# Kernel optimization log

Measured on AMD Instinct MI355X. Metric: run time of the kernel, lower is better.

## Reference

```python
import jax, jax.numpy as jnp
import numpy as np

NUM_HEADS = 12
LN_EPS = 1e-5


def _layernorm(x, w, b):
    m = jnp.mean(x, axis=-1, keepdims=True)
    v = jnp.mean(jnp.square(x - m), axis=-1, keepdims=True)
    return (x - m) * jax.lax.rsqrt(v + LN_EPS) * w + b


def setup_inputs() -> dict:
    key = jax.random.key(0)
    ks = jax.random.split(key, 6)
    B, N, C, H = 8, 1024, 768, 3072
    s = 0.02
    return {
        "x": jax.random.normal(ks[0], (B, N, C), jnp.float32),
        "ln1_w": jnp.ones((C,), jnp.float32),
        "ln1_b": jnp.zeros((C,), jnp.float32),
        "qkv_w": jax.random.normal(ks[1], (3 * C, C), jnp.float32) * s,
        "qkv_b": jnp.zeros((3 * C,), jnp.float32),
        "proj_w": jax.random.normal(ks[2], (C, C), jnp.float32) * s,
        "proj_b": jnp.zeros((C,), jnp.float32),
        "ln2_w": jnp.ones((C,), jnp.float32),
        "ln2_b": jnp.zeros((C,), jnp.float32),
        "fc1_w": jax.random.normal(ks[3], (H, C), jnp.float32) * s,
        "fc1_b": jnp.zeros((H,), jnp.float32),
        "fc2_w": jax.random.normal(ks[4], (C, H), jnp.float32) * s,
        "fc2_b": jnp.zeros((C,), jnp.float32),
    }


def reference(x, ln1_w, ln1_b, qkv_w, qkv_b, proj_w, proj_b,
              ln2_w, ln2_b, fc1_w, fc1_b, fc2_w, fc2_b):
    B, N, C = x.shape
    H = NUM_HEADS
    d = C // H
    scale = d ** (-0.5)

    # --- attention on norm1(x) (size=None path, dropout rates are 0) ---
    h = _layernorm(x, ln1_w, ln1_b)
    qkv = h @ qkv_w.T + qkv_b                      # [B,N,3C]
    qkv = qkv.reshape(B, N, 3, H, d).transpose(2, 0, 3, 1, 4)  # [3,B,H,N,d]
    q, k, v = qkv[0], qkv[1], qkv[2]
    attn = jnp.einsum('bhqd,bhkd->bhqk', q, k) * scale
    attn = jax.nn.softmax(attn, axis=-1)
    o = jnp.einsum('bhqk,bhkd->bhqd', attn, v)     # [B,H,N,d]
    o = o.transpose(0, 2, 1, 3).reshape(B, N, C)
    x_attn = o @ proj_w.T + proj_b

    # --- residual + MLP ---
    x = x + x_attn
    h2 = _layernorm(x, ln2_w, ln2_b)
    h2 = jax.nn.gelu(h2 @ fc1_w.T + fc1_b, approximate=False)
    x = x + (h2 @ fc2_w.T + fc2_b)
    return x
```

## Files before the change

### kernel.cpp

```cpp
#include <hip/hip_runtime.h>
#include <cmath>

typedef __bf16 bf16;
typedef __bf16 bf16x8 __attribute__((ext_vector_type(8)));
typedef __bf16 bf16x4 __attribute__((ext_vector_type(4)));
typedef float floatx4 __attribute__((ext_vector_type(4)));

#define MFMA16(A, B, C) __builtin_amdgcn_mfma_f32_16x16x32_bf16((A), (B), (C), 0, 0, 0)

#define GLDS16(g, l)                                                   \
  __builtin_amdgcn_global_load_lds(                                    \
      (const __attribute__((address_space(1))) void*)(g),              \
      (__attribute__((address_space(3))) void*)(l), 16, 0, 0)

__global__ __launch_bounds__(256) void pre_kernel(
    const float* __restrict__ x, const float* __restrict__ g,
    const float* __restrict__ be, bf16* __restrict__ h1,
    const float* __restrict__ s0, bf16* __restrict__ d0, int n0,
    const float* __restrict__ s1, bf16* __restrict__ d1, int n1,
    const float* __restrict__ s2, bf16* __restrict__ d2, int n2,
    const float* __restrict__ s3, bf16* __restrict__ d3, int n3) {
  int bid = blockIdx.x;
  int t = threadIdx.x;
  if (bid < 8192) {
    const float* xr = x + (size_t)bid * 768;
    float v0 = xr[t], v1 = xr[t + 256], v2 = xr[t + 512];
    float s = v0 + v1 + v2;
    float s2 = v0 * v0 + v1 * v1 + v2 * v2;
#pragma unroll
    for (int o = 1; o < 64; o <<= 1) {
      s += __shfl_xor(s, o, 64);
      s2 += __shfl_xor(s2, o, 64);
    }
    __shared__ float red[8];
    int w = t >> 6, lane = t & 63;
    if (lane == 0) { red[w] = s; red[4 + w] = s2; }
    __syncthreads();
    float ts = red[0] + red[1] + red[2] + red[3];
    float ts2 = red[4] + red[5] + red[6] + red[7];
    float mean = ts * (1.0f / 768.0f);
    float var = ts2 * (1.0f / 768.0f) - mean * mean;
    float rstd = rsqrtf(var + 1e-5f);
    bf16* orow = h1 + (size_t)bid * 768;
    orow[t]       = (bf16)((v0 - mean) * rstd * g[t]       + be[t]);
    orow[t + 256] = (bf16)((v1 - mean) * rstd * g[t + 256] + be[t + 256]);
    orow[t + 512] = (bf16)((v2 - mean) * rstd * g[t + 512] + be[t + 512]);
    return;
  }
  int i = (bid - 8192) * 256 + t;
  const float* s;
  bf16* d;
  if (i < n0) { s = s0 + (size_t)i * 4; d = d0 + (size_t)i * 4; }
  else if ((i -= n0) < n1) { s = s1 + (size_t)i * 4; d = d1 + (size_t)i * 4; }
  else if ((i -= n1) < n2) { s = s2 + (size_t)i * 4; d = d2 + (size_t)i * 4; }
  else if ((i -= n2) < n3) { s = s3 + (size_t)i * 4; d = d3 + (size_t)i * 4; }
  else return;
  bf16x4 v;
  v[0] = (bf16)s[0]; v[1] = (bf16)s[1]; v[2] = (bf16)s[2]; v[3] = (bf16)s[3];
  *(bf16x4*)d = v;
}

__global__ __launch_bounds__(256) void ln_kernel(const float* __restrict__ x,
                                                 const float* __restrict__ g,
                                                 const float* __restrict__ be,
                                                 bf16* __restrict__ out) {
  int row = blockIdx.x;
  int t = threadIdx.x;
  const float* xr = x + (size_t)row * 768;
  float v0 = xr[t], v1 = xr[t + 256], v2 = xr[t + 512];
  float s = v0 + v1 + v2;
  float s2 = v0 * v0 + v1 * v1 + v2 * v2;
#pragma unroll
  for (int o = 1; o < 64; o <<= 1) {
    s += __shfl_xor(s, o, 64);
    s2 += __shfl_xor(s2, o, 64);
  }
  __shared__ float red[8];
  int w = t >> 6, lane = t & 63;
  if (lane == 0) { red[w] = s; red[4 + w] = s2; }
  __syncthreads();
  float ts = red[0] + red[1] + red[2] + red[3];
  float ts2 = red[4] + red[5] + red[6] + red[7];
  float mean = ts * (1.0f / 768.0f);
  float var = ts2 * (1.0f / 768.0f) - mean * mean;
  float rstd = rsqrtf(var + 1e-5f);
  bf16* orow = out + (size_t)row * 768;
  orow[t]       = (bf16)((v0 - mean) * rstd * g[t]       + be[t]);
  orow[t + 256] = (bf16)((v1 - mean) * rstd * g[t + 256] + be[t + 256]);
  orow[t + 512] = (bf16)((v2 - mean) * rstd * g[t + 512] + be[t + 512]);
}

constexpr int EP_BF16 = 0;
constexpr int EP_RES_F32 = 1;
constexpr int EP_GELU_BF16 = 2;

template <int EP, int NJ>
__global__ __launch_bounds__(256, 3) void gemm_bt(
    const bf16* __restrict__ A, const bf16* __restrict__ Bw,
    const float* __restrict__ bias, const float* __restrict__ resid,
    void* __restrict__ outp, int M, int N, int K) {
  __shared__ alignas(16) bf16 Asl[128 * 64];
  __shared__ alignas(16) bf16 Bsl[NJ * 32 * 64];
  int tid = threadIdx.x;
  int lane = tid & 63, w = tid >> 6;
  int wm = w >> 1, wn = w & 1;
  int q16 = lane & 15, quad = lane >> 4;
  int fid = blockIdx.x + gridDim.x * blockIdx.y;
  int nb = gridDim.x;
  int s = fid >> 3;
  int m0 = ((fid & 7) * (gridDim.y >> 3) + s / nb) * 128;
  int n0 = (s % nb) * (NJ * 32);

  floatx4 acc[4][NJ];
#pragma unroll
  for (int i = 0; i < 4; i++)
#pragma unroll
    for (int j = 0; j < NJ; j++) acc[i][j] = (floatx4){0.f, 0.f, 0.f, 0.f};

  int rIn = lane >> 3;
  int cg = (lane & 7) ^ rIn;
  const bf16* ag[4];
  const bf16* bg[NJ];
#pragma unroll
  for (int q = 0; q < 4; q++)
    ag[q] = A + (size_t)(m0 + (w * 4 + q) * 8 + rIn) * K + cg * 8;
#pragma unroll
  for (int q = 0; q < NJ; q++)
    bg[q] = Bw + (size_t)(n0 + (w * NJ + q) * 8 + rIn) * K + cg * 8;
  bf16* la = &Asl[w * 2048];
  bf16* lb = &Bsl[w * NJ * 512];

  int msel = q16 & 7;
  int offA[2][4], offB[2][NJ];
#pragma unroll
  for (int ks = 0; ks < 2; ks++) {
#pragma unroll
    for (int i = 0; i < 4; i++)
      offA[ks][i] = (wm * 64 + i * 16 + q16) * 64 + (((ks * 4 + quad) ^ msel)) * 8;
#pragma unroll
    for (int j = 0; j < NJ; j++)
      offB[ks][j] = (wn * 16 * NJ + j * 16 + q16) * 64 + (((ks * 4 + quad) ^ msel)) * 8;
  }

  for (int k0 = 0; k0 < K; k0 += 64) {
    __syncthreads();
#pragma unroll
    for (int q = 0; q < 4; q++) {
      GLDS16(ag[q], la + q * 512);
      ag[q] += 64;
    }
#pragma unroll
    for (int q = 0; q < NJ; q++) {
      GLDS16(bg[q], lb + q * 512);
      bg[q] += 64;
    }
    __syncthreads();
#pragma unroll
    for (int ks = 0; ks < 2; ks++) {
      bf16x8 af[4], bfr[NJ];
#pragma unroll
      for (int i = 0; i < 4; i++) af[i] = *(const bf16x8*)&Asl[offA[ks][i]];
#pragma unroll
      for (int j = 0; j < NJ; j++) bfr[j] = *(const bf16x8*)&Bsl[offB[ks][j]];
#pragma unroll
      for (int i = 0; i < 4; i++)
#pragma unroll
        for (int j = 0; j < NJ; j++) acc[i][j] = MFMA16(af[i], bfr[j], acc[i][j]);
    }
  }

#pragma unroll
  for (int i = 0; i < 4; i++) {
#pragma unroll
    for (int j = 0; j < NJ; j++) {
#pragma unroll
      for (int r = 0; r < 4; r++) {
        int m = m0 + wm * 64 + i * 16 + quad * 4 + r;
        int n = n0 + wn * 16 * NJ + j * 16 + q16;
        size_t idx = (size_t)m * N + n;
        float v = acc[i][j][r] + bias[n];
        if constexpr (EP == EP_BF16) {
          ((bf16*)outp)[idx] = (bf16)v;
        } else if constexpr (EP == EP_RES_F32) {
          ((float*)outp)[idx] = v + resid[idx];
        } else {
          float u = v * (2.3022083f + 0.1029443f * v * v);
          float e = __builtin_amdgcn_exp2f(-u);
          float gv = v * __builtin_amdgcn_rcpf(1.0f + e);
          ((bf16*)outp)[idx] = (bf16)gv;
        }
      }
    }
  }
}

__global__ __launch_bounds__(256, 3) void attn_kernel(const bf16* __restrict__ qkv,
                                                      bf16* __restrict__ o) {
  __shared__ alignas(16) bf16 Kl[2][32 * 64];
  __shared__ alignas(16) bf16 Vt[2][64 * 40];
  __shared__ alignas(16) bf16 Pl[4][2][16 * 40];
  int tid = threadIdx.x;
  int lane = tid & 63, w = tid >> 6;
  int q16 = lane & 15, quad = lane >> 4;
  int b = blockIdx.y / 12, h = blockIdx.y % 12;
  int qbase = blockIdx.x * 128 + w * 32;
  const int KS = 32 * 2304;

  bf16x8 qf[2][2];
#pragma unroll
  for (int qt = 0; qt < 2; qt++)
#pragma unroll
    for (int c = 0; c < 2; c++)
      qf[qt][c] = *(const bf16x8*)(qkv +
          (size_t)(b * 1024 + qbase + qt * 16 + q16) * 2304 + h * 64 +
          c * 32 + quad * 8);

  int kkey = w * 8 + (lane >> 3);
  int kchunk = (lane & 7) ^ (lane >> 3);
  const bf16* kg = qkv + (size_t)(b * 1024 + kkey) * 2304 + 768 + h * 64 +
                   kchunk * 8;
  bf16* kd[2] = {&Kl[0][w * 512], &Kl[1][w * 512]};

  int kr = tid >> 3;
  int kcb = (tid & 7) * 8;
  const bf16* vg = qkv + (size_t)(b * 1024 + kr) * 2304 + 1536 + h * 64 + kcb;
  int vt_idx[8];
#pragma unroll
  for (int e = 0; e < 8; e++)
    vt_idx[e] = ((((kcb + e) * 5) + w) ^ (tid & 7)) * 8 + (kr & 7);

  int koff[2][2];
#pragma unroll
  for (int nc = 0; nc < 2; nc++)
#pragma unroll
    for (int ck = 0; ck < 2; ck++) {
      int key = nc * 16 + q16;
      koff[nc][ck] = (key * 8 + ((ck * 4 + quad) ^ (key & 7))) * 8;
    }
  int voff[4];
#pragma unroll
  for (int dc = 0; dc < 4; dc++) {
    int d = dc * 16 + q16;
    voff[dc] = ((d * 5 + quad) ^ ((d >> 3) & 7)) * 8;
  }
  const bf16* pread = &Pl[w][0][q16 * 40 + quad * 8];
  int pw_base = (quad * 4) * 40 + q16;

  float l_[2][4];
  floatx4 oacc[2][4];
#pragma unroll
  for (int qt = 0; qt < 2; qt++)
#pragma unroll
    for (int r = 0; r < 4; r++) l_[qt][r] = 0.f;
#pragma unroll
  for (int qt = 0; qt < 2; qt++)
#pragma unroll
    for (int dc = 0; dc < 4; dc++) oacc[qt][dc] = (floatx4){0.f, 0.f, 0.f, 0.f};

  GLDS16(kg, kd[0]);
  kg += KS;
  bf16x8 vv = *(const bf16x8*)vg;
  vg += KS;
#pragma unroll
  for (int e = 0; e < 8; e++) Vt[0][vt_idx[e]] = vv[e];
  vv = *(const bf16x8*)vg;
  vg += KS;

  for (int kt = 0; kt < 32; kt++) {
    int cur = kt & 1, nxt = cur ^ 1;
    __syncthreads();
    if (kt < 31) {
      GLDS16(kg, kd[nxt]);
      kg += KS;
#pragma unroll
      for (int e = 0; e < 8; e++) Vt[nxt][vt_idx[e]] = vv[e];
      if (kt < 30) {
        vv = *(const bf16x8*)vg;
        vg += KS;
      }
    }

    bf16x8 kf[2][2];
#pragma unroll
    for (int nc = 0; nc < 2; nc++)
#pragma unroll
      for (int ck = 0; ck < 2; ck++)
        kf[nc][ck] = *(const bf16x8*)&Kl[cur][koff[nc][ck]];

#pragma unroll
    for (int qt = 0; qt < 2; qt++) {
#pragma unroll
      for (int nc = 0; nc < 2; nc++) {
        floatx4 z = (floatx4){0.f, 0.f, 0.f, 0.f};
        z = MFMA16(qf[qt][0], kf[nc][0], z);
        z = MFMA16(qf[qt][1], kf[nc][1], z);
#pragma unroll
        for (int r = 0; r < 4; r++) {
          float p = __builtin_amdgcn_exp2f(z[r] * 0.18033688011f);
          l_[qt][r] += p;
          Pl[w][qt][pw_base + r * 40 + nc * 16] = (bf16)p;
        }
      }
    }

    bf16x8 vf[4];
#pragma unroll
    for (int dc = 0; dc < 4; dc++) vf[dc] = *(const bf16x8*)&Vt[cur][voff[dc]];
#pragma unroll
    for (int qt = 0; qt < 2; qt++) {
      bf16x8 pf = *(const bf16x8*)(pread + qt * 640);
#pragma unroll
      for (int dc = 0; dc < 4; dc++)
        oacc[qt][dc] = MFMA16(pf, vf[dc], oacc[qt][dc]);
    }
  }

#pragma unroll
  for (int qt = 0; qt < 2; qt++) {
    bf16* op = o + (size_t)(b * 1024 + qbase + qt * 16) * 768 + h * 64;
#pragma unroll
    for (int r = 0; r < 4; r++) {
      float s = l_[qt][r];
#pragma unroll
      for (int off = 1; off < 16; off <<= 1) s += __shfl_xor(s, off, 16);
      float inv = 1.0f / s;
#pragma unroll
      for (int dc = 0; dc < 4; dc++)
        op[(size_t)(quad * 4 + r) * 768 + dc * 16 + q16] =
            (bf16)(oacc[qt][dc][r] * inv);
    }
  }
}

extern "C" void kernel_launch(void* const* d_in, const int* in_sizes, int n_in,
                              void* d_out, int out_size, void* d_ws, size_t ws_size,
                              hipStream_t stream) {
  (void)in_sizes; (void)n_in; (void)out_size; (void)ws_size;
  const float* x      = (const float*)d_in[0];
  const float* ln1_w  = (const float*)d_in[1];
  const float* ln1_b  = (const float*)d_in[2];
  const float* qkv_w  = (const float*)d_in[3];
  const float* qkv_b  = (const float*)d_in[4];
  const float* proj_w = (const float*)d_in[5];
  const float* proj_b = (const float*)d_in[6];
  const float* ln2_w  = (const float*)d_in[7];
  const float* ln2_b  = (const float*)d_in[8];
  const float* fc1_w  = (const float*)d_in[9];
  const float* fc1_b  = (const float*)d_in[10];
  const float* fc2_w  = (const float*)d_in[11];
  const float* fc2_b  = (const float*)d_in[12];

  char* ws = (char*)d_ws;
  size_t off = 0;
  auto alloc = [&](size_t bytes) {
    void* p = ws + off;
    off += (bytes + 255) & ~(size_t)255;
    return p;
  };
  bf16* wq  = (bf16*)alloc((size_t)2304 * 768 * 2);
  bf16* wp  = (bf16*)alloc((size_t)768 * 768 * 2);
  bf16* wf1 = (bf16*)alloc((size_t)3072 * 768 * 2);
  bf16* wf2 = (bf16*)alloc((size_t)768 * 3072 * 2);
  bf16* slotA = (bf16*)alloc((size_t)8192 * 768 * 2);
  bf16* slotB = (bf16*)alloc((size_t)8192 * 3072 * 2);
  float* x1 = (float*)alloc((size_t)8192 * 768 * 4);

  bf16* h1 = slotA;
  bf16* qkvb = slotB;
  bf16* ob = slotA;
  bf16* h2 = slotA;
  bf16* hm = slotB;

  pre_kernel<<<8192 + 6912, 256, 0, stream>>>(
      x, ln1_w, ln1_b, h1,
      qkv_w, wq, 2304 * 768 / 4, proj_w, wp, 768 * 768 / 4,
      fc1_w, wf1, 3072 * 768 / 4, fc2_w, wf2, 768 * 3072 / 4);

  gemm_bt<EP_BF16, 4><<<dim3(18, 64), 256, 0, stream>>>(
      h1, wq, qkv_b, nullptr, qkvb, 8192, 2304, 768);
  attn_kernel<<<dim3(8, 96), 256, 0, stream>>>(qkvb, ob);
  gemm_bt<EP_RES_F32, 2><<<dim3(12, 64), 256, 0, stream>>>(
      ob, wp, proj_b, x, x1, 8192, 768, 768);
  ln_kernel<<<8192, 256, 0, stream>>>(x1, ln2_w, ln2_b, h2);
  gemm_bt<EP_GELU_BF16, 4><<<dim3(24, 64), 256, 0, stream>>>(
      h2, wf1, fc1_b, nullptr, hm, 8192, 3072, 768);
  gemm_bt<EP_RES_F32, 2><<<dim3(12, 64), 256, 0, stream>>>(
      hm, wf2, fc2_b, x1, (float*)d_out, 8192, 768, 3072);
}
```

Before: 321.2 us.

## Double-buffer LDS tiles in GEMM to overlap global loads with MFMA

Splits the GEMM's shared-memory A/B tiles into two buffers. The first K-tile is prefetched before the loop, and inside the loop the next tile is issued asynchronously with global_load_lds while MFMAs run on the current tile. This removes one barrier per iteration and is meant to hide global-memory latency behind compute. The cost is doubled LDS use, so the occupancy hint for NJ==4 drops from 3 to 2 blocks per CU, which may reduce latency hiding across waves.

Result: slower. 334.2 us (+4.1%).

```diff
diff --git a/kernel.cpp b/kernel.cpp
--- a/kernel.cpp
+++ b/kernel.cpp
@@ -95,12 +95,12 @@
 constexpr int EP_GELU_BF16 = 2;
 
 template <int EP, int NJ>
-__global__ __launch_bounds__(256, 3) void gemm_bt(
+__global__ __launch_bounds__(256, (NJ == 4 ? 2 : 3)) void gemm_bt(
     const bf16* __restrict__ A, const bf16* __restrict__ Bw,
     const float* __restrict__ bias, const float* __restrict__ resid,
     void* __restrict__ outp, int M, int N, int K) {
-  __shared__ alignas(16) bf16 Asl[128 * 64];
-  __shared__ alignas(16) bf16 Bsl[NJ * 32 * 64];
+  __shared__ alignas(16) bf16 Asl[2][128 * 64];
+  __shared__ alignas(16) bf16 Bsl[2][NJ * 32 * 64];
   int tid = threadIdx.x;
   int lane = tid & 63, w = tid >> 6;
   int wm = w >> 1, wn = w & 1;
@@ -127,8 +127,8 @@
 #pragma unroll
   for (int q = 0; q < NJ; q++)
     bg[q] = Bw + (size_t)(n0 + (w * NJ + q) * 8 + rIn) * K + cg * 8;
-  bf16* la = &Asl[w * 2048];
-  bf16* lb = &Bsl[w * NJ * 512];
+  bf16* la[2] = {&Asl[0][w * 2048], &Asl[1][w * 2048]};
+  bf16* lb[2] = {&Bsl[0][w * NJ * 512], &Bsl[1][w * NJ * 512]};
 
   int msel = q16 & 7;
   int offA[2][4], offB[2][NJ];
@@ -142,26 +142,43 @@
       offB[ks][j] = (wn * 16 * NJ + j * 16 + q16) * 64 + (((ks * 4 + quad) ^ msel)) * 8;
   }
 
-  for (int k0 = 0; k0 < K; k0 += 64) {
+#pragma unroll
+  for (int q = 0; q < 4; q++) {
+    GLDS16(ag[q], la[0] + q * 512);
+    ag[q] += 64;
+  }
+#pragma unroll
+  for (int q = 0; q < NJ; q++) {
+    GLDS16(bg[q], lb[0] + q * 512);
+    bg[q] += 64;
+  }
+
+  int nT = K >> 6;
+  for (int t = 0; t < nT; t++) {
+    int cur = t & 1;
     __syncthreads();
-#pragma unroll
-    for (int q = 0; q < 4; q++) {
-      GLDS16(ag[q], la + q * 512);
-      ag[q] += 64;
-    }
-#pragma unroll
-    for (int q = 0; q < NJ; q++) {
-      GLDS16(bg[q], lb + q * 512);
-      bg[q] += 64;
-    }
-    __syncthreads();
+    if (t + 1 < nT) {
+      int nxt = cur ^ 1;
+#pragma unroll
+      for (int q = 0; q < 4; q++) {
+        GLDS16(ag[q], la[nxt] + q * 512);
+        ag[q] += 64;
+      }
+#pragma unroll
+      for (int q = 0; q < NJ; q++) {
+        GLDS16(bg[q], lb[nxt] + q * 512);
+        bg[q] += 64;
+      }
+    }
+    const bf16* ab = Asl[cur];
+    const bf16* bb = Bsl[cur];
 #pragma unroll
     for (int ks = 0; ks < 2; ks++) {
       bf16x8 af[4], bfr[NJ];
 #pragma unroll
-      for (int i = 0; i < 4; i++) af[i] = *(const bf16x8*)&Asl[offA[ks][i]];
-#pragma unroll
-      for (int j = 0; j < NJ; j++) bfr[j] = *(const bf16x8*)&Bsl[offB[ks][j]];
+      for (int i = 0; i < 4; i++) af[i] = *(const bf16x8*)&ab[offA[ks][i]];
+#pragma unroll
+      for (int j = 0; j < NJ; j++) bfr[j] = *(const bf16x8*)&bb[offB[ks][j]];
 #pragma unroll
       for (int i = 0; i < 4; i++)
 #pragma unroll
```

## Keep attention probabilities in registers via transposed QK^T and lane shuffles; halve block size

Applied to the files above, without the earlier changes.

The attention kernel now computes S^T (K as the A operand), so each lane holds probabilities for one query across keys. It packs them to bf16 and redistributes them with cross-lane shuffles into the A-operand layout for the PV MFMA, dropping the shared-memory P buffer and its store/load round trip. Blocks shrink to 128 threads (2 waves, 64 queries) and the grid doubles, so each thread loads twice as much K and V per tile. Row sums are reduced once at the end. This adds shuffle instructions and more per-thread staging work.

Result: slower. 341.3 us (+6.3%).

```diff
diff --git a/kernel.cpp b/kernel.cpp
--- a/kernel.cpp
+++ b/kernel.cpp
@@ -4,6 +4,7 @@
 typedef __bf16 bf16;
 typedef __bf16 bf16x8 __attribute__((ext_vector_type(8)));
 typedef __bf16 bf16x4 __attribute__((ext_vector_type(4)));
+typedef __bf16 bf16x2 __attribute__((ext_vector_type(2)));
 typedef float floatx4 __attribute__((ext_vector_type(4)));
 
 #define MFMA16(A, B, C) __builtin_amdgcn_mfma_f32_16x16x32_bf16((A), (B), (C), 0, 0, 0)
@@ -12,6 +13,13 @@
   __builtin_amdgcn_global_load_lds(                                    \
       (const __attribute__((address_space(1))) void*)(g),              \
       (__attribute__((address_space(3))) void*)(l), 16, 0, 0)
+
+static __device__ __forceinline__ int pack2(float a, float b) {
+  bf16x2 t;
+  t[0] = (bf16)a;
+  t[1] = (bf16)b;
+  return __builtin_bit_cast(int, t);
+}
 
 __global__ __launch_bounds__(256) void pre_kernel(
     const float* __restrict__ x, const float* __restrict__ g,
@@ -194,16 +202,15 @@
   }
 }
 
-__global__ __launch_bounds__(256, 3) void attn_kernel(const bf16* __restrict__ qkv,
+__global__ __launch_bounds__(128, 3) void attn_kernel(const bf16* __restrict__ qkv,
                                                       bf16* __restrict__ o) {
   __shared__ alignas(16) bf16 Kl[2][32 * 64];
   __shared__ alignas(16) bf16 Vt[2][64 * 40];
-  __shared__ alignas(16) bf16 Pl[4][2][16 * 40];
   int tid = threadIdx.x;
   int lane = tid & 63, w = tid >> 6;
   int q16 = lane & 15, quad = lane >> 4;
   int b = blockIdx.y / 12, h = blockIdx.y % 12;
-  int qbase = blockIdx.x * 128 + w * 32;
+  int qbase = blockIdx.x * 64 + w * 32;
   const int KS = 32 * 2304;
 
   bf16x8 qf[2][2];
@@ -215,19 +222,25 @@
           (size_t)(b * 1024 + qbase + qt * 16 + q16) * 2304 + h * 64 +
           c * 32 + quad * 8);
 
-  int kkey = w * 8 + (lane >> 3);
-  int kchunk = (lane & 7) ^ (lane >> 3);
-  const bf16* kg = qkv + (size_t)(b * 1024 + kkey) * 2304 + 768 + h * 64 +
-                   kchunk * 8;
-  bf16* kd[2] = {&Kl[0][w * 512], &Kl[1][w * 512]};
-
-  int kr = tid >> 3;
-  int kcb = (tid & 7) * 8;
-  const bf16* vg = qkv + (size_t)(b * 1024 + kr) * 2304 + 1536 + h * 64 + kcb;
-  int vt_idx[8];
-#pragma unroll
-  for (int e = 0; e < 8; e++)
-    vt_idx[e] = ((((kcb + e) * 5) + w) ^ (tid & 7)) * 8 + (kr & 7);
+  int krow = lane >> 3;
+  int kchunk = (lane & 7) ^ krow;
+  const bf16* kg0 = qkv + (size_t)(b * 1024 + w * 16 + krow) * 2304 + 768 +
+                    h * 64 + kchunk * 8;
+  const bf16* kg1 = kg0 + 8 * 2304;
+  bf16* kdA[2] = {&Kl[0][w * 1024], &Kl[1][w * 1024]};
+
+  int kr = tid >> 2;
+  int dbase = (tid & 3) * 16;
+  const bf16* vgA = qkv + (size_t)(b * 1024 + kr) * 2304 + 1536 + h * 64 + dbase;
+  const bf16* vgB = vgA + 8;
+  int vtA[8], vtB[8];
+#pragma unroll
+  for (int e = 0; e < 8; e++) {
+    int dA = dbase + e;
+    int dB = dbase + 8 + e;
+    vtA[e] = ((dA * 5 + (kr >> 3)) ^ ((dA >> 3) & 7)) * 8 + (kr & 7);
+    vtB[e] = ((dB * 5 + (kr >> 3)) ^ ((dB >> 3) & 7)) * 8 + (kr & 7);
+  }
 
   int koff[2][2];
 #pragma unroll
@@ -243,40 +256,47 @@
     int d = dc * 16 + q16;
     voff[dc] = ((d * 5 + quad) ^ ((d >> 3) & 7)) * 8;
   }
-  const bf16* pread = &Pl[w][0][q16 * 40 + quad * 8];
-  int pw_base = (quad * 4) * 40 + q16;
-
-  float l_[2][4];
+
+  int srcLo = q16 + ((quad & 1) << 5);
+  int srcHi = srcLo + 16;
+  bool loH = quad < 2;
+
+  float lsum[2] = {0.f, 0.f};
   floatx4 oacc[2][4];
 #pragma unroll
   for (int qt = 0; qt < 2; qt++)
 #pragma unroll
-    for (int r = 0; r < 4; r++) l_[qt][r] = 0.f;
-#pragma unroll
-  for (int qt = 0; qt < 2; qt++)
-#pragma unroll
     for (int dc = 0; dc < 4; dc++) oacc[qt][dc] = (floatx4){0.f, 0.f, 0.f, 0.f};
 
-  GLDS16(kg, kd[0]);
-  kg += KS;
-  bf16x8 vv = *(const bf16x8*)vg;
-  vg += KS;
-#pragma unroll
-  for (int e = 0; e < 8; e++) Vt[0][vt_idx[e]] = vv[e];
-  vv = *(const bf16x8*)vg;
-  vg += KS;
+  GLDS16(kg0, kdA[0]);
+  GLDS16(kg1, kdA[0] + 512);
+  kg0 += KS; kg1 += KS;
+  bf16x8 va = *(const bf16x8*)vgA;
+  bf16x8 vb = *(const bf16x8*)vgB;
+  vgA += KS; vgB += KS;
+#pragma unroll
+  for (int e = 0; e < 8; e++) Vt[0][vtA[e]] = va[e];
+#pragma unroll
+  for (int e = 0; e < 8; e++) Vt[0][vtB[e]] = vb[e];
+  va = *(const bf16x8*)vgA;
+  vb = *(const bf16x8*)vgB;
+  vgA += KS; vgB += KS;
 
   for (int kt = 0; kt < 32; kt++) {
     int cur = kt & 1, nxt = cur ^ 1;
     __syncthreads();
     if (kt < 31) {
-      GLDS16(kg, kd[nxt]);
-      kg += KS;
-#pragma unroll
-      for (int e = 0; e < 8; e++) Vt[nxt][vt_idx[e]] = vv[e];
+      GLDS16(kg0, kdA[nxt]);
+      GLDS16(kg1, kdA[nxt] + 512);
+      kg0 += KS; kg1 += KS;
+#pragma unroll
+      for (int e = 0; e < 8; e++) Vt[nxt][vtA[e]] = va[e];
+#pragma unroll
+      for (int e = 0; e < 8; e++) Vt[nxt][vtB[e]] = vb[e];
       if (kt < 30) {
-        vv = *(const bf16x8*)vg;
-        vg += KS;
+        va = *(const bf16x8*)vgA;
+        vb = *(const bf16x8*)vgB;
+        vgA += KS; vgB += KS;
       }
     }
 
@@ -286,48 +306,58 @@
 #pragma unroll
       for (int ck = 0; ck < 2; ck++)
         kf[nc][ck] = *(const bf16x8*)&Kl[cur][koff[nc][ck]];
+    bf16x8 vf[4];
+#pragma unroll
+    for (int dc = 0; dc < 4; dc++) vf[dc] = *(const bf16x8*)&Vt[cur][voff[dc]];
 
 #pragma unroll
     for (int qt = 0; qt < 2; qt++) {
-#pragma unroll
-      for (int nc = 0; nc < 2; nc++) {
-        floatx4 z = (floatx4){0.f, 0.f, 0.f, 0.f};
-        z = MFMA16(qf[qt][0], kf[nc][0], z);
-        z = MFMA16(qf[qt][1], kf[nc][1], z);
-#pragma unroll
-        for (int r = 0; r < 4; r++) {
-          float p = __builtin_amdgcn_exp2f(z[r] * 0.18033688011f);
-          l_[qt][r] += p;
-          Pl[w][qt][pw_base + r * 40 + nc * 16] = (bf16)p;
-        }
+      floatx4 z0 = (floatx4){0.f, 0.f, 0.f, 0.f};
+      floatx4 z1 = (floatx4){0.f, 0.f, 0.f, 0.f};
+      z0 = MFMA16(kf[0][0], qf[qt][0], z0);
+      z0 = MFMA16(kf[0][1], qf[qt][1], z0);
+      z1 = MFMA16(kf[1][0], qf[qt][0], z1);
+      z1 = MFMA16(kf[1][1], qf[qt][1], z1);
+      float e0[4], e1[4];
+#pragma unroll
+      for (int r = 0; r < 4; r++) {
+        e0[r] = __builtin_amdgcn_exp2f(z0[r] * 0.18033688011f);
+        e1[r] = __builtin_amdgcn_exp2f(z1[r] * 0.18033688011f);
+        lsum[qt] += e0[r] + e1[r];
       }
-    }
-
-    bf16x8 vf[4];
-#pragma unroll
-    for (int dc = 0; dc < 4; dc++) vf[dc] = *(const bf16x8*)&Vt[cur][voff[dc]];
-#pragma unroll
-    for (int qt = 0; qt < 2; qt++) {
-      bf16x8 pf = *(const bf16x8*)(pread + qt * 640);
+      int A0 = pack2(e0[0], e0[1]);
+      int A1 = pack2(e0[2], e0[3]);
+      int B0 = pack2(e1[0], e1[1]);
+      int B1 = pack2(e1[2], e1[3]);
+      int tA0 = __shfl(A0, srcLo, 64), tB0 = __shfl(B0, srcLo, 64);
+      int tA1 = __shfl(A1, srcLo, 64), tB1 = __shfl(B1, srcLo, 64);
+      int tA2 = __shfl(A0, srcHi, 64), tB2 = __shfl(B0, srcHi, 64);
+      int tA3 = __shfl(A1, srcHi, 64), tB3 = __shfl(B1, srcHi, 64);
+      union { int i[4]; bf16x8 v; } pu;
+      pu.i[0] = loH ? tA0 : tB0;
+      pu.i[1] = loH ? tA1 : tB1;
+      pu.i[2] = loH ? tA2 : tB2;
+      pu.i[3] = loH ? tA3 : tB3;
 #pragma unroll
       for (int dc = 0; dc < 4; dc++)
-        oacc[qt][dc] = MFMA16(pf, vf[dc], oacc[qt][dc]);
+        oacc[qt][dc] = MFMA16(pu.v, vf[dc], oacc[qt][dc]);
     }
   }
 
 #pragma unroll
   for (int qt = 0; qt < 2; qt++) {
+    float s = lsum[qt];
+    s += __shfl_xor(s, 16, 64);
+    s += __shfl_xor(s, 32, 64);
+    float inv = 1.0f / s;
     bf16* op = o + (size_t)(b * 1024 + qbase + qt * 16) * 768 + h * 64;
 #pragma unroll
     for (int r = 0; r < 4; r++) {
-      float s = l_[qt][r];
-#pragma unroll
-      for (int off = 1; off < 16; off <<= 1) s += __shfl_xor(s, off, 16);
-      float inv = 1.0f / s;
+      float invr = __shfl(inv, quad * 4 + r, 64);
 #pragma unroll
       for (int dc = 0; dc < 4; dc++)
         op[(size_t)(quad * 4 + r) * 768 + dc * 16 + q16] =
-            (bf16)(oacc[qt][dc][r] * inv);
+            (bf16)(oacc[qt][dc][r] * invr);
     }
   }
 }
@@ -378,7 +408,7 @@
 
   gemm_bt<EP_BF16, 4><<<dim3(18, 64), 256, 0, stream>>>(
       h1, wq, qkv_b, nullptr, qkvb, 8192, 2304, 768);
-  attn_kernel<<<dim3(8, 96), 256, 0, stream>>>(qkvb, ob);
+  attn_kernel<<<dim3(16, 96), 128, 0, stream>>>(qkvb, ob);
   gemm_bt<EP_RES_F32, 2><<<dim3(12, 64), 256, 0, stream>>>(
       ob, wp, proj_b, x, x1, 8192, 768, 768);
   ln_kernel<<<8192, 256, 0, stream>>>(x1, ln2_w, ln2_b, h2);
```
